# Performance work log

Measured on AMD Instinct MI355X. Metric: run time of the kernel, lower is better.

## Reference

```python
import jax, jax.numpy as jnp
import numpy as np

T, N, D, V = 512, 256, 1024, 128000  # total tokens, sampled tokens, d_model, vocab


def setup_inputs() -> dict:
    key = jax.random.key(0)
    k1, k2, k3, k4, k5 = jax.random.split(key, 5)
    hidden_states = jax.random.normal(k1, (T, D), dtype=jnp.float32)
    embedding = jax.random.normal(k2, (V, D), dtype=jnp.float32) * 0.02
    # temperatures in [0.5, 1.5): realistic, avoids divide blow-up (0.0 maps to 1.0 in source)
    temperatures = 0.5 + jax.random.uniform(k3, (N,), dtype=jnp.float32)
    # top_p in [0.5, 1.0)
    top_ps = 0.5 + 0.5 * jax.random.uniform(k4, (N,), dtype=jnp.float32)
    last_token_indices = jnp.sort(jax.random.randint(k5, (N,), 0, T))
    return {
        "hidden_states": hidden_states,
        "embedding": embedding,
        "temperatures": temperatures,
        "top_ps": top_ps,
        "last_token_indices": last_token_indices,
    }


def reference(hidden_states, embedding, temperatures, top_ps, last_token_indices):
    # gather last-token hidden states, project to vocab logits
    h = hidden_states[last_token_indices]              # [N, D]
    logits = jnp.einsum("nd,vd->nv", h, embedding)     # [N, V]
    # temperature softmax
    probs = jax.nn.softmax(logits / temperatures[:, None], axis=-1)
    # top-p: descending sort, cumsum, mask tail, renormalize, un-sort
    order = jnp.argsort(-probs, axis=-1)               # descending order indices
    probs_sort = jnp.take_along_axis(probs, order, axis=-1)
    cum = jnp.cumsum(probs_sort, axis=-1)
    mask = (cum - probs_sort) > top_ps[:, None]
    probs_sort = jnp.where(mask, 0.0, probs_sort)
    probs_sort = probs_sort / jnp.sum(probs_sort, axis=-1, keepdims=True)
    inv = jnp.argsort(order, axis=-1)                  # inverse permutation
    probs_f = jnp.take_along_axis(probs_sort, inv, axis=-1)
    # multinomial sampling (one token per row), fixed key for determinism
    tokens = jax.random.categorical(jax.random.key(42), jnp.log(probs_f + 1e-20), axis=-1)
    return probs_f, tokens
```

## Files before the change

kernel.cpp:

```cpp
#include <hip/hip_runtime.h>
#include <stdint.h>

#define N_TOK 256
#define D_MODEL 1024
#define VOCAB 128000
#define NV_ELEMS (256LL * 128000LL)
#define LIST_CAP 24576
#define TIE_ALL 0xFFFFFFFFu

typedef unsigned long long u64;
typedef uint32_t u32;
typedef __attribute__((ext_vector_type(8))) short bfrag;
typedef __attribute__((ext_vector_type(4))) float facc;

__device__ __forceinline__ uint32_t bf16_rne_bits(float x) {
    uint32_t u = __float_as_uint(x);
    return (u + 0x7fffu + ((u >> 16) & 1u)) >> 16;
}

__device__ __forceinline__ uint32_t rotl32(uint32_t x, int d) {
    return (x << d) | (x >> (32 - d));
}

__device__ __forceinline__ u32 mono32(u32 b) {
    return (b & 0x80000000u) ? ~b : (b | 0x80000000u);
}
__device__ __forceinline__ float unmono32(u32 k) {
    u32 b = (k & 0x80000000u) ? (k & 0x7FFFFFFFu) : ~k;
    return __uint_as_float(b);
}

__device__ __forceinline__ u64 fixmass(float rv) {
    return (u64)(rv * 1073741824.0f);
}

__device__ __forceinline__ uint2 tf_0_42(uint32_t c0, uint32_t c1) {
    const uint32_t ks0 = 0u, ks1 = 42u, ks2 = 0x1BD11BDAu ^ 42u;
    uint32_t x0 = c0 + ks0, x1 = c1 + ks1;
#define R4(a,b,c,d) \
    x0 += x1; x1 = rotl32(x1,a); x1 ^= x0; \
    x0 += x1; x1 = rotl32(x1,b); x1 ^= x0; \
    x0 += x1; x1 = rotl32(x1,c); x1 ^= x0; \
    x0 += x1; x1 = rotl32(x1,d); x1 ^= x0;
    R4(13,15,26,6)   x0 += ks1; x1 += ks2 + 1u;
    R4(17,29,16,24)  x0 += ks2; x1 += ks0 + 2u;
    R4(13,15,26,6)   x0 += ks0; x1 += ks1 + 3u;
    R4(17,29,16,24)  x0 += ks1; x1 += ks2 + 4u;
    R4(13,15,26,6)   x0 += ks2; x1 += ks0 + 5u;
#undef R4
    return make_uint2(x0, x1);
}

__device__ __forceinline__ uint32_t jax_bits(uint32_t j) {
    uint2 r = tf_0_42(0u, j);
    return r.x ^ r.y;
}

__device__ __forceinline__ float jax_gumbel(uint32_t bits) {
    const float TINY = 1.17549435e-38f;
    float u = __uint_as_float((bits >> 9) | 0x3f800000u) - 1.0f;
    u = u + TINY;
    u = fmaxf(TINY, u);
    return -__logf(-__logf(u));
}

__device__ __forceinline__ float rv_of(float l, float rinv) {
    return __expf(l * rinv);
}

__device__ __forceinline__ void async_copy16(const void* g, void* lbase, int lane) {
#if defined(__has_builtin) && __has_builtin(__builtin_amdgcn_global_load_lds)
    __builtin_amdgcn_global_load_lds((const uint32_t*)g, (uint32_t*)lbase, 16, 0, 0);
#else
    *(bfrag*)((char*)lbase + lane * 16) = *(const bfrag*)g;
#endif
}

__device__ __forceinline__ void scan_desc_u64(const u64* h, int nb, u64 carry, u64 P,
                                              int* outCb, u64* outSa) {
    int lane = (int)threadIdx.x & 63;
    int chunk = nb >> 6;
    int top = nb - 1 - lane * chunk;
    u64 ls = 0ull;
    for (int j = 0; j < chunk; ++j) ls += h[top - j];
    u64 incl = ls;
    for (int o = 1; o < 64; o <<= 1) {
        u64 v = __shfl_up(incl, o, 64);
        if (lane >= o) incl += v;
    }
    u64 s0 = carry + incl - ls;
    unsigned long long mask = __ballot(s0 + ls > P);
    if (mask == 0ull) {
        if (lane == 0) { *outCb = 0; *outSa = carry; }
    } else {
        int cstar = (int)__builtin_ctzll(mask);
        if (lane == cstar) {
            u64 sa = s0; int cb = 0;
            for (int j = 0; j < chunk; ++j) {
                int b = top - j;
                if (sa + h[b] > P) { cb = b; break; }
                sa += h[b];
            }
            *outCb = cb; *outSa = sa;
        }
    }
}

__global__ __launch_bounds__(256) void prep_a(
        const float* __restrict__ hidden, const int* __restrict__ idx,
        ushort* __restrict__ wsA) {
    const int m = blockIdx.x;
    const int t = threadIdx.x;
    const float* src = hidden + (long long)idx[m] * D_MODEL;
    const uint32_t swz = (uint32_t)((m & 7) << 4);
    for (int j = 0; j < 4; ++j) {
        int k = t * 4 + j;
        float x = src[k];
        uint32_t hb = bf16_rne_bits(x);
        float hf = __uint_as_float(hb << 16);
        uint32_t lb = bf16_rne_bits(x - hf);
        int kt = k >> 5, kk = k & 31, g = kk >> 3, e = kk & 7;
        char* img = (char*)wsA + (size_t)kt * 32768;
        uint32_t base = (uint32_t)(m * 128 + g * 32);
        *(ushort*)(img + ((base + 0) ^ swz) + e * 2) = (ushort)hb;
        *(ushort*)(img + ((base + 16) ^ swz) + e * 2) = (ushort)lb;
    }
}

__global__ __launch_bounds__(256) void gemm_mfma(
        const ushort* __restrict__ wsA, const float* __restrict__ emb,
        float* __restrict__ logits) {
    __shared__ __align__(16) ushort Aimg[16384];
    __shared__ __align__(16) ushort Bimg[4096];
    const int tid = (int)threadIdx.x;
    const int w = tid >> 6, l = tid & 63;
    const int lr = l & 15, lg = l >> 4;
    const int v0 = blockIdx.x * 64;
    char* Ab = (char*)Aimg;
    char* Bb = (char*)Bimg;

    facc acc[4][4] = {};

    for (int kt = 0; kt < 32; ++kt) {
        __syncthreads();
        const char* asrc = (const char*)wsA + (size_t)kt * 32768;
#pragma unroll
        for (int i = 0; i < 8; ++i) {
            int off = w * 8192 + i * 1024;
            async_copy16(asrc + off + l * 16, Ab + off, l);
        }
        {
            int rb = tid >> 2, g = tid & 3;
            const float* bs = emb + (size_t)(v0 + rb) * D_MODEL + kt * 32 + g * 8;
            float4 x0 = *(const float4*)bs;
            float4 x1 = *(const float4*)(bs + 4);
            float xs[8] = {x0.x, x0.y, x0.z, x0.w, x1.x, x1.y, x1.z, x1.w};
            bfrag h, lo;
#pragma unroll
            for (int e = 0; e < 8; ++e) {
                uint32_t hb = bf16_rne_bits(xs[e]);
                float hf = __uint_as_float(hb << 16);
                uint32_t lb = bf16_rne_bits(xs[e] - hf);
                h[e] = (short)hb; lo[e] = (short)lb;
            }
            uint32_t swz = (uint32_t)((rb & 7) << 4);
            uint32_t base = (uint32_t)(rb * 128 + g * 32);
            *(bfrag*)(Bb + ((base + 0) ^ swz)) = h;
            *(bfrag*)(Bb + ((base + 16) ^ swz)) = lo;
        }
        __syncthreads();
        bfrag bh[4], bl[4];
#pragma unroll
        for (int nj = 0; nj < 4; ++nj) {
            int rb = nj * 16 + lr;
            uint32_t swz = (uint32_t)((rb & 7) << 4);
            uint32_t base = (uint32_t)(rb * 128 + lg * 32);
            bh[nj] = *(const bfrag*)(Bb + ((base + 0) ^ swz));
            bl[nj] = *(const bfrag*)(Bb + ((base + 16) ^ swz));
        }
#pragma unroll
        for (int mi = 0; mi < 4; ++mi) {
            int r = w * 64 + mi * 16 + lr;
            uint32_t swz = (uint32_t)((r & 7) << 4);
            uint32_t base = (uint32_t)(r * 128 + lg * 32);
            bfrag ah = *(const bfrag*)(Ab + ((base + 0) ^ swz));
            bfrag al = *(const bfrag*)(Ab + ((base + 16) ^ swz));
#pragma unroll
            for (int nj = 0; nj < 4; ++nj) {
                acc[mi][nj] = __builtin_amdgcn_mfma_f32_16x16x32_bf16(ah, bh[nj], acc[mi][nj], 0, 0, 0);
                acc[mi][nj] = __builtin_amdgcn_mfma_f32_16x16x32_bf16(ah, bl[nj], acc[mi][nj], 0, 0, 0);
                acc[mi][nj] = __builtin_amdgcn_mfma_f32_16x16x32_bf16(al, bh[nj], acc[mi][nj], 0, 0, 0);
            }
        }
    }
#pragma unroll
    for (int mi = 0; mi < 4; ++mi) {
        int mbase = w * 64 + mi * 16 + lg * 4;
#pragma unroll
        for (int nj = 0; nj < 4; ++nj) {
            int v = v0 + nj * 16 + lr;
#pragma unroll
            for (int reg = 0; reg < 4; ++reg)
                logits[(size_t)(mbase + reg) * VOCAB + v] = acc[mi][nj][reg];
        }
    }
}

__global__ __launch_bounds__(256) void gemm_kernel(
        const float* __restrict__ hidden, const int* __restrict__ idx,
        const float* __restrict__ emb, float* __restrict__ logits) {
    __shared__ float As[16][64];
    __shared__ float Bs[16][64];
    const int n0 = blockIdx.x * 64, v0 = blockIdx.y * 64;
    const int tid = threadIdx.x;
    const int tx = tid & 15, ty = tid >> 4;
    const int lr = tid >> 2, lk = (tid & 3) * 4;
    float acc[4][4] = {};
    const long long aRow = (long long)idx[n0 + lr] * D_MODEL + lk;
    const long long bRow = (long long)(v0 + lr) * D_MODEL + lk;
    for (int k0 = 0; k0 < D_MODEL; k0 += 16) {
        float4 av = *(const float4*)(hidden + aRow + k0);
        float4 bv = *(const float4*)(emb + bRow + k0);
        __syncthreads();
        As[lk + 0][lr] = av.x; As[lk + 1][lr] = av.y; As[lk + 2][lr] = av.z; As[lk + 3][lr] = av.w;
        Bs[lk + 0][lr] = bv.x; Bs[lk + 1][lr] = bv.y; Bs[lk + 2][lr] = bv.z; Bs[lk + 3][lr] = bv.w;
        __syncthreads();
#pragma unroll
        for (int kk = 0; kk < 16; ++kk) {
            float4 a = *(const float4*)&As[kk][ty * 4];
            float4 b = *(const float4*)&Bs[kk][tx * 4];
            float aa[4] = {a.x, a.y, a.z, a.w};
            float bb[4] = {b.x, b.y, b.z, b.w};
#pragma unroll
            for (int i = 0; i < 4; ++i)
#pragma unroll
                for (int j = 0; j < 4; ++j)
                    acc[i][j] += aa[i] * bb[j];
        }
    }
#pragma unroll
    for (int i = 0; i < 4; ++i) {
        float4 o = make_float4(acc[i][0], acc[i][1], acc[i][2], acc[i][3]);
        *(float4*)(logits + (long long)(n0 + ty * 4 + i) * VOCAB + (v0 + tx * 4)) = o;
    }
}

__global__ __launch_bounds__(1024) void resolveC_kernel(
        const float* __restrict__ probs, const float* __restrict__ temps,
        const float* __restrict__ topps,
        u32* __restrict__ scTs, u32* __restrict__ scTieN,
        float* __restrict__ scInvSp, u32* __restrict__ tieKept,
        u64* __restrict__ argmax) {
    const int row = blockIdx.x, tid = (int)threadIdx.x;
    __shared__ u64 h1[4096];
    __shared__ u32 c3[1024];
    __shared__ u32 tlist[1024];
    __shared__ u64 wredu[16];
    __shared__ int sCb; __shared__ u64 sSa;
    __shared__ u64 sP;
    __shared__ u32 sTc, sTsKey, sMt, sCntb;
    __shared__ float sInv;

    const float rinv = 1.0f / temps[row];
    const float4* R4 = (const float4*)(probs + (size_t)row * VOCAB);

    for (int i = tid; i < 4096; i += 1024) h1[i] = 0ull;
    __syncthreads();
    for (int i = 0; i < 32; ++i) {
        int j = tid + i * 1024;
        if (j < 32000) {
            float4 x = R4[j];
            float xs[4] = {x.x, x.y, x.z, x.w};
#pragma unroll
            for (int c = 0; c < 4; ++c) {
                u32 key = mono32(__float_as_uint(xs[c]));
                atomicAdd(&h1[key >> 20], fixmass(rv_of(xs[c], rinv)));
            }
        }
    }
    __syncthreads();
    {
        u64 s = h1[tid] + h1[tid + 1024] + h1[tid + 2048] + h1[tid + 3072];
        for (int o = 32; o >= 1; o >>= 1) s += __shfl_xor(s, o, 64);
        if ((tid & 63) == 0) wredu[tid >> 6] = s;
    }
    __syncthreads();
    if (tid == 0) {
        u64 S = 0ull;
        for (int w2 = 0; w2 < 16; ++w2) S += wredu[w2];
        sP = (u64)((double)topps[row] * (double)S);
    }
    __syncthreads();
    const u64 P = sP;
    if (tid < 64) scan_desc_u64(h1, 4096, 0ull, P, &sCb, &sSa);
    __syncthreads();
    const u32 cb1 = (u32)sCb; const u64 carry1 = sSa;
    __syncthreads();

    h1[tid] = 0ull;
    __syncthreads();
    for (int i = 0; i < 32; ++i) {
        int j = tid + i * 1024;
        if (j < 32000) {
            float4 x = R4[j];
            float xs[4] = {x.x, x.y, x.z, x.w};
#pragma unroll
            for (int c = 0; c < 4; ++c) {
                u32 key = mono32(__float_as_uint(xs[c]));
                if ((key >> 20) == cb1)
                    atomicAdd(&h1[(key >> 10) & 1023u], fixmass(rv_of(xs[c], rinv)));
            }
        }
    }
    __syncthreads();
    if (tid < 64) scan_desc_u64(h1, 1024, carry1, P, &sCb, &sSa);
    __syncthreads();
    const u32 cb2 = (u32)sCb; const u64 carry2 = sSa;
    __syncthreads();

    const u32 pref2 = (cb1 << 10) | cb2;
    h1[tid] = 0ull; c3[tid] = 0u;
    __syncthreads();
    for (int i = 0; i < 32; ++i) {
        int j = tid + i * 1024;
        if (j < 32000) {
            float4 x = R4[j];
            float xs[4] = {x.x, x.y, x.z, x.w};
#pragma unroll
            for (int c = 0; c < 4; ++c) {
                u32 key = mono32(__float_as_uint(xs[c]));
                if ((key >> 10) == pref2) {
                    atomicAdd(&h1[key & 1023u], fixmass(rv_of(xs[c], rinv)));
                    atomicAdd(&c3[key & 1023u], 1u);
                }
            }
        }
    }
    __syncthreads();
    if (tid < 64) scan_desc_u64(h1, 1024, carry2, P, &sCb, &sSa);
    __syncthreads();
    if (tid == 0) {
        const int cb3 = sCb; const u64 sa3 = sSa;
        u32 ts = (pref2 << 10) | (u32)cb3;
        u32 cntb = c3[cb3]; if (cntb == 0u) cntb = 1u;
        u64 tfq = fixmass(rv_of(unmono32(ts), rinv));
        u64 rem = P - sa3;
        u32 mt;
        if (tfq == 0ull) mt = cntb;
        else {
            u64 q = rem / tfq;
            mt = (q >= (u64)(cntb - 1)) ? cntb : ((u32)q + 1u);
        }
        u64 Spq = sa3 + (u64)mt * tfq;
        sTsKey = ts; sMt = mt; sCntb = cntb;
        sInv = (float)(1073741824.0 / (double)Spq);
        sTc = 0u;
    }
    __syncthreads();
    const u32 ts = sTsKey, mt = sMt, cntb = sCntb;

    if (mt < cntb) {
        for (int i = 0; i < 32; ++i) {
            int j = tid + i * 1024;
            if (j < 32000) {
                float4 x = R4[j];
                float xs[4] = {x.x, x.y, x.z, x.w};
#pragma unroll
                for (int c = 0; c < 4; ++c) {
                    u32 key = mono32(__float_as_uint(xs[c]));
                    if (key == ts) {
                        u32 pos = atomicAdd(&sTc, 1u);
                        if (pos < 1024u) tlist[pos] = (u32)(j * 4 + c);
                    }
                }
            }
        }
        __syncthreads();
        const u32 tn = min(sTc, 1024u);
        if ((u32)tid < tn) {
            u32 my = tlist[tid];
            u32 rank = 0;
            for (u32 j2 = 0; j2 < tn; ++j2) rank += (tlist[j2] < my) ? 1u : 0u;
            if (rank < mt) tieKept[(size_t)row * 1024 + rank] = my;
        }
        if (tid == 0) scTieN[row] = min(mt, tn);
    } else {
        if (tid == 0) scTieN[row] = TIE_ALL;
    }
    if (tid == 0) {
        scTs[row] = ts;
        scInvSp[row] = sInv;
        argmax[row] = 0ull;
    }
}

__global__ __launch_bounds__(512) void final2_kernel(
        float* __restrict__ probs, const float* __restrict__ temps,
        const u32* __restrict__ scTs, const u32* __restrict__ scTieN,
        const float* __restrict__ scInvSp, const u32* __restrict__ tieKept,
        u64* __restrict__ argmax) {
    const int row = blockIdx.y, hb = blockIdx.x, tid = (int)threadIdx.x;
    __shared__ u32 tl[1024];
    __shared__ u64 wbest[8];
    const u32 ts = scTs[row], tieN = scTieN[row];
    const u32 tlN = (tieN == TIE_ALL) ? 0u : tieN;
    const float invSp = scInvSp[row];
    const float rinv = 1.0f / temps[row];
    for (u32 i = tid; i < tlN; i += 512) tl[i] = tieKept[(size_t)row * 1024 + i];
    __syncthreads();
    float4* R4 = (float4*)(probs + (size_t)row * VOCAB);
    const u32 rowBase = (u32)row * (u32)VOCAB;
    const int base4 = hb * 8000;
    u64 best = 0ull;
    for (int i = 0; i < 16; ++i) {
        int j = tid + i * 512;
        if (j < 8000) {
            float4 x = R4[base4 + j];
            float xs[4] = {x.x, x.y, x.z, x.w};
            float4 out;
            float* op = (float*)&out;
#pragma unroll
            for (int c = 0; c < 4; ++c) {
                u32 key = mono32(__float_as_uint(xs[c]));
                u32 v = (u32)((base4 + j) * 4 + c);
                bool kept = key > ts;
                if (key == ts) {
                    if (tieN == TIE_ALL) {
                        kept = true;
                    } else {
                        kept = false;
                        for (u32 q2 = 0; q2 < tlN; ++q2)
                            if (tl[q2] == v) { kept = true; break; }
                    }
                }
                if (kept) {
                    float pf = rv_of(xs[c], rinv) * invSp;
                    op[c] = pf;
                    float g = jax_gumbel(jax_bits(rowBase + v));
                    float val = __logf(pf + 1e-20f) + g;
                    u64 pk = ((u64)mono32(__float_as_uint(val)) << 32) | (u32)(~v);
                    if (pk > best) best = pk;
                } else {
                    op[c] = 0.0f;
                }
            }
            R4[base4 + j] = out;
        }
    }
    for (int o = 32; o >= 1; o >>= 1) {
        u64 ob = __shfl_xor(best, o, 64);
        if (ob > best) best = ob;
    }
    if ((tid & 63) == 0) wbest[tid >> 6] = best;
    __syncthreads();
    if (tid == 0) {
        u64 b = wbest[0];
        for (int w2 = 1; w2 < 8; ++w2) if (wbest[w2] > b) b = wbest[w2];
        atomicMax(&argmax[row], b);
    }
}

__global__ void token_kernel(const u64* __restrict__ argmax, float* __restrict__ outTok) {
    int n = (int)threadIdx.x;
    if (n < N_TOK) outTok[n] = (float)(~(u32)argmax[n]);
}

__device__ __forceinline__ void scan_desc_wave(const float* h, int nb, float carry,
                                               float P, int* outCb, float* outSa) {
    int lane = (int)threadIdx.x & 63;
    int chunk = nb >> 6;
    int top = nb - 1 - lane * chunk;
    float ls = 0.0f;
    for (int j = 0; j < chunk; ++j) ls += h[top - j];
    float incl = ls;
    for (int o = 1; o < 64; o <<= 1) {
        float v = __shfl_up(incl, o, 64);
        if (lane >= o) incl += v;
    }
    float s0 = carry + incl - ls;
    unsigned long long mask = __ballot(s0 + ls > P);
    if (mask == 0ull) {
        if (lane == 63) { *outCb = 0; *outSa = carry + incl - h[0]; }
    } else {
        int cstar = (int)__builtin_ctzll(mask);
        if (lane == cstar) {
            float sa = s0; int cb = 0;
            for (int j = 0; j < chunk; ++j) {
                int b = top - j;
                if (sa + h[b] > P) { cb = b; break; }
                sa += h[b];
            }
            *outCb = cb; *outSa = sa;
        }
    }
}

__global__ __launch_bounds__(1024) void sample_kernel(
        float* __restrict__ probs, const float* __restrict__ temps,
        const float* __restrict__ topps, float* __restrict__ outTok) {
    const int row = blockIdx.x;
    const int tid = (int)threadIdx.x;
    float* L = probs + (long long)row * VOCAB;
    const float4* L4 = (const float4*)L;
    float4* L4w = (float4*)L;

    __shared__ float waveH[16][2048];
    __shared__ float hsum[2048];
    __shared__ uint32_t hcnt[1024];
    __shared__ float wred[16];
    __shared__ float aVal[16];
    __shared__ int aIdx[16];
    __shared__ uint32_t tieList[256];
    __shared__ int sCb;
    __shared__ float sSa;
    __shared__ float sP, sCarry1, sCarry2, sSp, sInvSp;
    __shared__ uint32_t sPref1, sCb2, sTsKey, sMt, sTieN, sCnt;
    uint32_t* keys = (uint32_t*)&waveH[4][0];

    const float t = temps[row];
    const float p = topps[row];
    const float rinv = 1.0f / t;

    for (int i = tid; i < 16 * 2048; i += 1024) ((float*)waveH)[i] = 0.0f;
    __syncthreads();
    {
        float* myH = waveH[tid >> 6];
#pragma unroll 2
        for (int i = 0; i < 31; ++i) {
            float4 x = L4[tid + i * 1024];
            float r0 = rv_of(x.x, rinv), r1 = rv_of(x.y, rinv);
            float r2 = rv_of(x.z, rinv), r3 = rv_of(x.w, rinv);
            atomicAdd(&myH[__float_as_uint(r0) >> 20], r0);
            atomicAdd(&myH[__float_as_uint(r1) >> 20], r1);
            atomicAdd(&myH[__float_as_uint(r2) >> 20], r2);
            atomicAdd(&myH[__float_as_uint(r3) >> 20], r3);
        }
        if (tid < 256) {
            float4 x = L4[31744 + tid];
            float r0 = rv_of(x.x, rinv), r1 = rv_of(x.y, rinv);
            float r2 = rv_of(x.z, rinv), r3 = rv_of(x.w, rinv);
            atomicAdd(&myH[__float_as_uint(r0) >> 20], r0);
            atomicAdd(&myH[__float_as_uint(r1) >> 20], r1);
            atomicAdd(&myH[__float_as_uint(r2) >> 20], r2);
            atomicAdd(&myH[__float_as_uint(r3) >> 20], r3);
        }
    }
    __syncthreads();
    {
        float a0 = 0.0f, a1 = 0.0f;
#pragma unroll
        for (int w2 = 0; w2 < 16; ++w2) { a0 += waveH[w2][tid]; a1 += waveH[w2][tid + 1024]; }
        hsum[tid] = a0; hsum[tid + 1024] = a1;
        float s = a0 + a1;
        for (int o = 32; o >= 1; o >>= 1) s += __shfl_xor(s, o, 64);
        if ((tid & 63) == 0) wred[tid >> 6] = s;
    }
    __syncthreads();
    if (tid == 0) {
        float tot = 0.0f;
        for (int w2 = 0; w2 < 16; ++w2) tot += wred[w2];
        sP = p * tot;
    }
    __syncthreads();
    if (tid < 64) scan_desc_wave(hsum, 2048, 0.0f, sP, &sCb, &sSa);
    __syncthreads();
    if (tid == 0) { sPref1 = (uint32_t)sCb; sCarry1 = sSa; sCnt = 0u; }
    __syncthreads();

    const uint32_t pref1 = sPref1;
    const float P = sP;
#pragma unroll 2
    for (int i = 0; i < 31; ++i) {
        float4 x = L4[tid + i * 1024];
        float rr[4] = {rv_of(x.x, rinv), rv_of(x.y, rinv), rv_of(x.z, rinv), rv_of(x.w, rinv)};
#pragma unroll
        for (int c = 0; c < 4; ++c) {
            uint32_t key = __float_as_uint(rr[c]);
            if ((key >> 20) == pref1) {
                uint32_t pos = atomicAdd(&sCnt, 1u);
                if (pos < LIST_CAP) keys[pos] = key;
            }
        }
    }
    if (tid < 256) {
        float4 x = L4[31744 + tid];
        float rr[4] = {rv_of(x.x, rinv), rv_of(x.y, rinv), rv_of(x.z, rinv), rv_of(x.w, rinv)};
#pragma unroll
        for (int c = 0; c < 4; ++c) {
            uint32_t key = __float_as_uint(rr[c]);
            if ((key >> 20) == pref1) {
                uint32_t pos = atomicAdd(&sCnt, 1u);
                if (pos < LIST_CAP) keys[pos] = key;
            }
        }
    }
    __syncthreads();
    const uint32_t K = sCnt;
    const bool inLds = (K <= LIST_CAP);

    if (tid < 1024) hsum[tid] = 0.0f;
    __syncthreads();
    if (inLds) {
        for (uint32_t j = tid; j < K; j += 1024) {
            uint32_t key = keys[j];
            atomicAdd(&hsum[(key >> 10) & 1023u], __uint_as_float(key));
        }
    } else {
        for (int i = 0; i < 125; ++i) {
            int v = tid + i * 1024;
            float rv = rv_of(L[v], rinv);
            uint32_t key = __float_as_uint(rv);
            if ((key >> 20) == pref1) atomicAdd(&hsum[(key >> 10) & 1023u], rv);
        }
    }
    __syncthreads();
    if (tid < 64) scan_desc_wave(hsum, 1024, sCarry1, P, &sCb, &sSa);
    __syncthreads();
    if (tid == 0) { sCb2 = (uint32_t)sCb; sCarry2 = sSa; }
    __syncthreads();

    const uint32_t cb2 = sCb2;
    if (tid < 1024) { hsum[tid] = 0.0f; hcnt[tid] = 0u; }
    __syncthreads();
    if (inLds) {
        for (uint32_t j = tid; j < K; j += 1024) {
            uint32_t key = keys[j];
            if (((key >> 10) & 1023u) == cb2) {
                atomicAdd(&hsum[key & 1023u], __uint_as_float(key));
                atomicAdd(&hcnt[key & 1023u], 1u);
            }
        }
    } else {
        const uint32_t pref2full = (pref1 << 10) | cb2;
        for (int i = 0; i < 125; ++i) {
            int v = tid + i * 1024;
            float rv = rv_of(L[v], rinv);
            uint32_t key = __float_as_uint(rv);
            if ((key >> 10) == pref2full) {
                atomicAdd(&hsum[key & 1023u], rv);
                atomicAdd(&hcnt[key & 1023u], 1u);
            }
        }
    }
    __syncthreads();
    if (tid < 64) scan_desc_wave(hsum, 1024, sCarry2, P, &sCb, &sSa);
    __syncthreads();
    if (tid == 0) {
        int cb3 = sCb; float sa3 = sSa;
        uint32_t ts = (pref1 << 20) | (cb2 << 10) | (uint32_t)cb3;
        uint32_t cnt = hcnt[cb3]; if (cnt == 0u) cnt = 1u;
        float tf = __uint_as_float(ts);
        uint32_t mt;
        float rem = P - sa3; if (rem < 0.0f) rem = 0.0f;
        if (!(tf > 0.0f)) mt = cnt;
        else {
            float q = floorf(rem / tf);
            mt = (q >= (float)(cnt - 1)) ? cnt : ((uint32_t)q + 1u);
        }
        sTsKey = ts; sMt = mt;
        sSp = sa3 + (float)mt * tf;
        sInvSp = 1.0f / sSp;
        sTieN = 0u;
    }
    __syncthreads();

    const uint32_t ts = sTsKey, mt = sMt;
    const float invSp = sInvSp;
    float bestV = -INFINITY;
    int bestI = 0x7FFFFFFF;
    const uint32_t rowBase = (uint32_t)row * (uint32_t)VOCAB;
    for (int i = 0; i < 32; ++i) {
        int f4i = (i < 31) ? (tid + i * 1024) : (31744 + tid);
        if (i == 31 && tid >= 256) break;
        float4 x = L4[f4i];
        float rr[4] = {rv_of(x.x, rinv), rv_of(x.y, rinv), rv_of(x.z, rinv), rv_of(x.w, rinv)};
        float4 out;
        float* op = (float*)&out;
#pragma unroll
        for (int c = 0; c < 4; ++c) {
            uint32_t key = __float_as_uint(rr[c]);
            int v = f4i * 4 + c;
            if (key > ts) {
                float pf = rr[c] * invSp;
                op[c] = pf;
                float g = jax_gumbel(jax_bits(rowBase + (uint32_t)v));
                float val = __logf(pf + 1e-20f) + g;
                if (val > bestV || (val == bestV && v < bestI)) { bestV = val; bestI = v; }
            } else if (key == ts) {
                op[c] = 0.0f;
                uint32_t pos = atomicAdd(&sTieN, 1u);
                if (pos < 256u) tieList[pos] = (uint32_t)v;
            } else {
                op[c] = 0.0f;
            }
        }
        L4w[f4i] = out;
    }
    __syncthreads();
    {
        const uint32_t tn = min(sTieN, 256u);
        if ((uint32_t)tid < tn) {
            uint32_t v = tieList[tid];
            uint32_t rank = 0;
            for (uint32_t j = 0; j < tn; ++j) rank += (tieList[j] < v) ? 1u : 0u;
            if (rank < mt) {
                float pf = __uint_as_float(ts) * invSp;
                L[v] = pf;
                float g = jax_gumbel(jax_bits(rowBase + v));
                float val = __logf(pf + 1e-20f) + g;
                if (val > bestV || (val == bestV && (int)v < bestI)) { bestV = val; bestI = (int)v; }
            }
        }
    }
    for (int o = 32; o >= 1; o >>= 1) {
        float ov = __shfl_xor(bestV, o, 64);
        int oi = __shfl_xor(bestI, o, 64);
        if (ov > bestV || (ov == bestV && oi < bestI)) { bestV = ov; bestI = oi; }
    }
    if ((tid & 63) == 0) { aVal[tid >> 6] = bestV; aIdx[tid >> 6] = bestI; }
    __syncthreads();
    if (tid == 0) {
        float bv = aVal[0]; int bi = aIdx[0];
        for (int w2 = 1; w2 < 16; ++w2) {
            if (aVal[w2] > bv || (aVal[w2] == bv && aIdx[w2] < bi)) { bv = aVal[w2]; bi = aIdx[w2]; }
        }
        outTok[row] = (float)bi;
    }
}

extern "C" void kernel_launch(void* const* d_in, const int* in_sizes, int n_in,
                              void* d_out, int out_size, void* d_ws, size_t ws_size,
                              hipStream_t stream) {
    const float* hidden = (const float*)d_in[0];
    const float* emb    = (const float*)d_in[1];
    const float* temps  = (const float*)d_in[2];
    const float* topps  = (const float*)d_in[3];
    const int*   idx    = (const int*)d_in[4];

    float* probs  = (float*)d_out;
    float* outTok = probs + NV_ELEMS;

    char* ws = (char*)d_ws;
    const bool wsGemm = ws_size >= (size_t)(1u << 20);
    const bool wsBig  = ws_size >= (size_t)(4u << 20);

    if (wsGemm) {
        ushort* wsA = (ushort*)ws;
        prep_a<<<N_TOK, 256, 0, stream>>>(hidden, idx, wsA);
        gemm_mfma<<<VOCAB / 64, 256, 0, stream>>>(wsA, emb, probs);
    } else {
        gemm_kernel<<<dim3(4, 2000), 256, 0, stream>>>(hidden, idx, emb, probs);
    }

    if (wsBig) {
        char* m        = ws + (2u << 20);
        u32* scTs      = (u32*)(m);
        u32* scTieN    = (u32*)(m + 1024);
        float* scInvSp = (float*)(m + 2048);
        u64* argmax    = (u64*)(m + 3072);
        u32* tieKept   = (u32*)(m + 8192);

        resolveC_kernel<<<N_TOK, 1024, 0, stream>>>(probs, temps, topps,
                                                    scTs, scTieN, scInvSp,
                                                    tieKept, argmax);
        final2_kernel<<<dim3(4, N_TOK), 512, 0, stream>>>(probs, temps, scTs, scTieN,
                                                          scInvSp, tieKept, argmax);
        token_kernel<<<1, 256, 0, stream>>>(argmax, outTok);
    } else {
        sample_kernel<<<N_TOK, 1024, 0, stream>>>(probs, temps, topps, outTok);
    }
}
```

Before: 434.0 us.

## Replicate first-level histogram and cache candidate keys in LDS for third pass

The first radix-select histogram pass now spreads its atomics over four LDS replicas, chosen by wave, which are summed afterwards to cut atomic contention on the few hot bins. During the second pass, keys that fall in the selected top bin are compacted into an LDS list with wave-ballot allocation. The third pass then scans that list instead of re-reading the whole 128000-element row from global memory, and falls back to the full scan if the list overflows. In exchange the kernel uses much more shared memory (128KB), which may limit occupancy, and adds ballot and compaction work to the second pass.

```diff
diff --git a/kernel.cpp b/kernel.cpp
--- a/kernel.cpp
+++ b/kernel.cpp
@@ -6,6 +6,7 @@
 #define VOCAB 128000
 #define NV_ELEMS (256LL * 128000LL)
 #define LIST_CAP 24576
+#define KCAP 24576
 #define TIE_ALL 0xFFFFFFFFu
 
 typedef unsigned long long u64;
@@ -252,37 +253,49 @@
         float* __restrict__ scInvSp, u32* __restrict__ tieKept,
         u64* __restrict__ argmax) {
     const int row = blockIdx.x, tid = (int)threadIdx.x;
-    __shared__ u64 h1[4096];
-    __shared__ u32 c3[1024];
+    __shared__ u64 hrep[4][4096];
     __shared__ u32 tlist[1024];
     __shared__ u64 wredu[16];
     __shared__ int sCb; __shared__ u64 sSa;
     __shared__ u64 sP;
-    __shared__ u32 sTc, sTsKey, sMt, sCntb;
+    __shared__ u32 sCb1; __shared__ u64 sCarry1;
+    __shared__ u32 sCb2; __shared__ u64 sCarry2;
+    __shared__ u32 sListCnt, sTc, sTsKey, sMt, sCntb;
     __shared__ float sInv;
+
+    u32* klist = (u32*)&hrep[0][0];
+    u64* h2    = (u64*)((char*)&hrep[0][0] + 98304);
+    u32* c3    = (u32*)((char*)&hrep[0][0] + 106496);
 
     const float rinv = 1.0f / temps[row];
     const float4* R4 = (const float4*)(probs + (size_t)row * VOCAB);
-
-    for (int i = tid; i < 4096; i += 1024) h1[i] = 0ull;
-    __syncthreads();
-    for (int i = 0; i < 32; ++i) {
-        int j = tid + i * 1024;
-        if (j < 32000) {
-            float4 x = R4[j];
-            float xs[4] = {x.x, x.y, x.z, x.w};
-#pragma unroll
-            for (int c = 0; c < 4; ++c) {
-                u32 key = mono32(__float_as_uint(xs[c]));
-                atomicAdd(&h1[key >> 20], fixmass(rv_of(xs[c], rinv)));
-            }
-        }
-    }
+    const int lane = tid & 63;
+
+    for (int i = tid; i < 16384; i += 1024) ((u64*)hrep)[i] = 0ull;
     __syncthreads();
     {
-        u64 s = h1[tid] + h1[tid + 1024] + h1[tid + 2048] + h1[tid + 3072];
+        u64* myrep = hrep[(tid >> 6) & 3];
+        for (int i = 0; i < 32; ++i) {
+            int j = tid + i * 1024;
+            if (j < 32000) {
+                float4 x = R4[j];
+                float xs[4] = {x.x, x.y, x.z, x.w};
+#pragma unroll
+                for (int c = 0; c < 4; ++c) {
+                    u32 key = mono32(__float_as_uint(xs[c]));
+                    atomicAdd(&myrep[key >> 20], fixmass(rv_of(xs[c], rinv)));
+                }
+            }
+        }
+    }
+    __syncthreads();
+    for (int b = tid; b < 4096; b += 1024)
+        hrep[0][b] += hrep[1][b] + hrep[2][b] + hrep[3][b];
+    __syncthreads();
+    {
+        u64 s = hrep[0][tid] + hrep[0][tid + 1024] + hrep[0][tid + 2048] + hrep[0][tid + 3072];
         for (int o = 32; o >= 1; o >>= 1) s += __shfl_xor(s, o, 64);
-        if ((tid & 63) == 0) wredu[tid >> 6] = s;
+        if (lane == 0) wredu[tid >> 6] = s;
     }
     __syncthreads();
     if (tid == 0) {
@@ -292,52 +305,75 @@
     }
     __syncthreads();
     const u64 P = sP;
-    if (tid < 64) scan_desc_u64(h1, 4096, 0ull, P, &sCb, &sSa);
-    __syncthreads();
-    const u32 cb1 = (u32)sCb; const u64 carry1 = sSa;
-    __syncthreads();
-
-    h1[tid] = 0ull;
-    __syncthreads();
+    if (tid < 64) scan_desc_u64(hrep[0], 4096, 0ull, P, &sCb, &sSa);
+    __syncthreads();
+    if (tid == 0) { sCb1 = (u32)sCb; sCarry1 = sSa; sListCnt = 0u; }
+    __syncthreads();
+    const u32 cb1 = sCb1;
+    h2[tid] = 0ull; c3[tid] = 0u;
+    __syncthreads();
+
     for (int i = 0; i < 32; ++i) {
         int j = tid + i * 1024;
-        if (j < 32000) {
-            float4 x = R4[j];
-            float xs[4] = {x.x, x.y, x.z, x.w};
-#pragma unroll
-            for (int c = 0; c < 4; ++c) {
-                u32 key = mono32(__float_as_uint(xs[c]));
-                if ((key >> 20) == cb1)
-                    atomicAdd(&h1[(key >> 10) & 1023u], fixmass(rv_of(xs[c], rinv)));
-            }
-        }
-    }
-    __syncthreads();
-    if (tid < 64) scan_desc_u64(h1, 1024, carry1, P, &sCb, &sSa);
-    __syncthreads();
-    const u32 cb2 = (u32)sCb; const u64 carry2 = sSa;
-    __syncthreads();
-
+        bool valid = j < 32000;
+        float4 x = valid ? R4[j] : make_float4(0.f, 0.f, 0.f, 0.f);
+        float xs[4] = {x.x, x.y, x.z, x.w};
+#pragma unroll
+        for (int c = 0; c < 4; ++c) {
+            u32 key = mono32(__float_as_uint(xs[c]));
+            bool m = valid && ((key >> 20) == cb1);
+            if (m) atomicAdd(&h2[(key >> 10) & 1023u], fixmass(rv_of(xs[c], rinv)));
+            unsigned long long grp = __ballot(m);
+            if (m) {
+                u32 prefix = (u32)__popcll(grp & ((1ull << lane) - 1ull));
+                int leader = (int)__builtin_ctzll(grp);
+                u32 base = 0u;
+                if (lane == leader) base = atomicAdd(&sListCnt, (u32)__popcll(grp));
+                base = (u32)__shfl((int)base, leader, 64);
+                u32 pos = base + prefix;
+                if (pos < KCAP) klist[pos] = key;
+            }
+        }
+    }
+    __syncthreads();
+    const u32 listTotal = sListCnt;
+    const bool inLds = listTotal <= (u32)KCAP;
+    if (tid < 64) scan_desc_u64(h2, 1024, sCarry1, P, &sCb, &sSa);
+    __syncthreads();
+    if (tid == 0) { sCb2 = (u32)sCb; sCarry2 = sSa; }
+    __syncthreads();
+    const u32 cb2 = sCb2;
     const u32 pref2 = (cb1 << 10) | cb2;
-    h1[tid] = 0ull; c3[tid] = 0u;
-    __syncthreads();
-    for (int i = 0; i < 32; ++i) {
-        int j = tid + i * 1024;
-        if (j < 32000) {
-            float4 x = R4[j];
-            float xs[4] = {x.x, x.y, x.z, x.w};
-#pragma unroll
-            for (int c = 0; c < 4; ++c) {
-                u32 key = mono32(__float_as_uint(xs[c]));
-                if ((key >> 10) == pref2) {
-                    atomicAdd(&h1[key & 1023u], fixmass(rv_of(xs[c], rinv)));
-                    atomicAdd(&c3[key & 1023u], 1u);
+    h2[tid] = 0ull; c3[tid] = 0u;
+    __syncthreads();
+
+    if (inLds) {
+        for (u32 q = tid; q < listTotal; q += 1024) {
+            u32 key = klist[q];
+            if ((key >> 10) == pref2) {
+                atomicAdd(&h2[key & 1023u], fixmass(rv_of(unmono32(key), rinv)));
+                atomicAdd(&c3[key & 1023u], 1u);
+            }
+        }
+    } else {
+        for (int i = 0; i < 32; ++i) {
+            int j = tid + i * 1024;
+            if (j < 32000) {
+                float4 x = R4[j];
+                float xs[4] = {x.x, x.y, x.z, x.w};
+#pragma unroll
+                for (int c = 0; c < 4; ++c) {
+                    u32 key = mono32(__float_as_uint(xs[c]));
+                    if ((key >> 10) == pref2) {
+                        atomicAdd(&h2[key & 1023u], fixmass(rv_of(xs[c], rinv)));
+                        atomicAdd(&c3[key & 1023u], 1u);
+                    }
                 }
             }
         }
     }
     __syncthreads();
-    if (tid < 64) scan_desc_u64(h1, 1024, carry2, P, &sCb, &sSa);
+    if (tid < 64) scan_desc_u64(h2, 1024, sCarry2, P, &sCb, &sSa);
     __syncthreads();
     if (tid == 0) {
         const int cb3 = sCb; const u64 sa3 = sSa;
```

After: 430.0 us. No clear change (-0.9%).
